# Optimization experiments

Measured on AMD Instinct MI355X. Metric: run time of the kernel, lower is better.

The kernel has to match this reference:

```python
import jax, jax.numpy as jnp
import numpy as np

C = 256
CQK = C // 8  # query/key channels


def setup_inputs() -> dict:
    key = jax.random.key(0)
    ks = jax.random.split(key, 7)
    B, H, W = 4, 64, 64
    x = jax.random.normal(ks[0], (B, C, H, W), dtype=jnp.float32)
    # 1x1 conv weights stored as [out_ch, in_ch] (kernel spatial dims are 1)
    sc = 1.0 / np.sqrt(C)
    Wq = jax.random.uniform(ks[1], (CQK, C), jnp.float32, -sc, sc)
    bq = jax.random.uniform(ks[2], (CQK,), jnp.float32, -sc, sc)
    Wk = jax.random.uniform(ks[3], (CQK, C), jnp.float32, -sc, sc)
    bk = jax.random.uniform(ks[4], (CQK,), jnp.float32, -sc, sc)
    Wv = jax.random.uniform(ks[5], (C, C), jnp.float32, -sc, sc)
    bv = jax.random.uniform(ks[6], (C,), jnp.float32, -sc, sc)
    gamma = jnp.zeros((1,), dtype=jnp.float32)
    return {"x": x, "Wq": Wq, "bq": bq, "Wk": Wk, "bk": bk, "Wv": Wv, "bv": bv, "gamma": gamma}


def reference(x, Wq, bq, Wk, bk, Wv, bv, gamma):
    B, Ch, H, W = x.shape
    N = H * W
    xf = x.reshape(B, Ch, N)  # [B, C, N]
    # 1x1 convs == per-pixel linear projections
    q = jnp.einsum('oc,bcn->bno', Wq, xf) + bq  # [B, N, CQK]
    k = jnp.einsum('oc,bcn->bon', Wk, xf) + bk[None, :, None]  # [B, CQK, N]
    v = jnp.einsum('oc,bcn->bon', Wv, xf) + bv[None, :, None]  # [B, C, N]
    s = jnp.einsum('bnd,bdm->bnm', q, k)  # [B, N, N]
    attn = jax.nn.softmax(s, axis=-1)
    # out[b,c,i] = sum_j v[b,c,j] * attn[b,i,j]
    out = jnp.einsum('bcj,bij->bci', v, attn).reshape(B, Ch, H, W)
    return x + gamma[0] * out
```

## Files before the change

kernel.cpp:

```cpp
#include <hip/hip_runtime.h>
#include <math.h>

#define BATCH 4
#define CCH   256
#define DQK   32
#define NPIX  4096
#define LOG2E 1.44269504088896340736f

typedef __attribute__((ext_vector_type(8)))  short          short8_t;
typedef __attribute__((ext_vector_type(4)))  unsigned short ushort4_t;
typedef __attribute__((ext_vector_type(8)))  unsigned short ushort8_t;
typedef __attribute__((ext_vector_type(16))) float          f32x16;
typedef __attribute__((ext_vector_type(2)))  unsigned int   uint2_t;

#if __has_builtin(__builtin_amdgcn_exp2f)
#define EXP2F(x) __builtin_amdgcn_exp2f(x)
#else
#define EXP2F(x) exp2f(x)
#endif

#define MFMA32(a, b, c) __builtin_amdgcn_mfma_f32_32x32x16_bf16(a, b, c, 0, 0, 0)

static __device__ __forceinline__ unsigned short f2bf(float f) {
    union { float f; unsigned int u; } v; v.f = f;
    unsigned int r = v.u + 0x7FFFu + ((v.u >> 16) & 1u);
    return (unsigned short)(r >> 16);
}

static __device__ __forceinline__ short8_t cat8(ushort4_t a, ushort4_t b) {
    ushort8_t c = __builtin_shufflevector(a, b, 0, 1, 2, 3, 4, 5, 6, 7);
    short8_t r; __builtin_memcpy(&r, &c, 16); return r;
}

static __device__ __forceinline__ short8_t u4_to_s8(const unsigned int* u) {
    short8_t r; __builtin_memcpy(&r, u, 16); return r;
}

static __device__ __forceinline__ uint2_t plswap(unsigned int a, unsigned int b) {
#if __has_builtin(__builtin_amdgcn_permlane32_swap)
    return __builtin_amdgcn_permlane32_swap(a, b, false, false);
#else
    const unsigned int sa = (unsigned int)__shfl_xor((int)a, 32);
    const unsigned int sb = (unsigned int)__shfl_xor((int)b, 32);
    const int h = (threadIdx.x >> 5) & 1;
    uint2_t r;
    r.x = h ? sb : a;
    r.y = h ? b : sa;
    return r;
#endif
}

static __device__ __forceinline__ void make_bfrag(
    const f32x16& s, float& l0, float& l1, unsigned int bfr[2][4])
{
    float pv[16];
    #pragma unroll
    for (int r = 0; r < 16; ++r) pv[r] = EXP2F(s[r]);
    #pragma unroll
    for (int r = 0; r < 16; r += 2) { l0 += pv[r]; l1 += pv[r + 1]; }
    unsigned int P[8];
    #pragma unroll
    for (int v = 0; v < 8; ++v)
        P[v] = __builtin_amdgcn_perm(__float_as_uint(pv[2 * v + 1]),
                                     __float_as_uint(pv[2 * v]), 0x07060302u);
    #pragma unroll
    for (int kp = 0; kp < 2; ++kp) {
        const uint2_t r02 = plswap(P[4 * kp + 0], P[4 * kp + 2]);
        const uint2_t r13 = plswap(P[4 * kp + 1], P[4 * kp + 3]);
        bfr[kp][0] = r02.x; bfr[kp][1] = r13.x;
        bfr[kp][2] = r02.y; bfr[kp][3] = r13.y;
    }
}

__global__ __launch_bounds__(256) void wconv_kernel(
    const float* __restrict__ Wq, const float* __restrict__ Wk,
    const float* __restrict__ Wv, unsigned short* __restrict__ wbf)
{
    const int idx = blockIdx.x * 256 + threadIdx.x;
    const int o = idx >> 8, c = idx & 255;
    float v;
    if (o < 32)      v = Wq[o * 256 + c] * LOG2E;
    else if (o < 64) v = Wk[(o - 32) * 256 + c];
    else             v = Wv[(o - 64) * 256 + c];
    wbf[((c >> 3) * 320 + o) * 8 + (c & 7)] = f2bf(v);
}

__global__ __launch_bounds__(256) void xt_kernel(
    const float* __restrict__ x, unsigned short* __restrict__ xfrag)
{
    const int b  = blockIdx.x >> 6;
    const int cg = (blockIdx.x >> 4) & 3;
    const int ng = blockIdx.x & 15;
    const int t  = threadIdx.x;
    const int w = t >> 6, l = t & 63;

    #pragma unroll
    for (int sgl = 0; sgl < 2; ++sgl) {
        const int sg = w * 2 + sgl;
        float f[4][8];
        #pragma unroll
        for (int p = 0; p < 8; ++p) {
            const float* row = x + ((size_t)(b * CCH + cg * 64 + sg * 8 + p)) * NPIX
                                 + ng * 256;
            #pragma unroll
            for (int j = 0; j < 4; ++j)
                f[j][p] = row[j * 64 + l];
        }
        #pragma unroll
        for (int j = 0; j < 4; ++j) {
            unsigned int d[4];
            #pragma unroll
            for (int k = 0; k < 4; ++k)
                d[k] = __builtin_amdgcn_perm(__float_as_uint(f[j][2 * k + 1]),
                                             __float_as_uint(f[j][2 * k]), 0x07060302u);
            const int nt = ng * 8 + j * 2 + (l >> 5);
            unsigned short* dst = xfrag +
                ((((size_t)(b * 128 + nt) * 32) + cg * 8 + sg) * 32 + (l & 31)) * 8;
            *(short8_t*)dst = u4_to_s8(d);
        }
    }
}

__global__ __launch_bounds__(320) void proj_kernel(
    const unsigned short* __restrict__ xfrag, const unsigned short* __restrict__ wbf,
    const float* __restrict__ bq, const float* __restrict__ bk,
    const float* __restrict__ bv,
    unsigned short* __restrict__ qfrag, unsigned short* __restrict__ kfrag,
    unsigned short* __restrict__ vfrag)
{
    __shared__ unsigned short qkb[2 * 2 * 32 * 40];
    __shared__ unsigned short vbuf[4 * 64 * 72];

    const int b   = blockIdx.x >> 6;
    const int nt0 = (blockIdx.x & 63) << 1;
    const int t   = threadIdx.x;
    const int w = t >> 6, lane = t & 63, il = lane & 31, h = lane >> 5;

    float4 bA[4], bB[4];
    #pragma unroll
    for (int g = 0; g < 4; ++g) {
        if (w == 0) {
            bA[g] = *(const float4*)&bq[8 * g + 4 * h];
            bB[g] = *(const float4*)&bk[8 * g + 4 * h];
        } else {
            bA[g] = *(const float4*)&bv[(w - 1) * 64 + 8 * g + 4 * h];
            bB[g] = *(const float4*)&bv[(w - 1) * 64 + 32 + 8 * g + 4 * h];
        }
    }

    f32x16 acc[2][2];
    #pragma unroll
    for (int a = 0; a < 2; ++a)
        #pragma unroll
        for (int i = 0; i < 2; ++i)
            #pragma unroll
            for (int r = 0; r < 16; ++r) acc[a][i][r] = 0.f;

    const unsigned short* wp = wbf + ((size_t)(h * 320 + w * 64 + il)) * 8;
    const unsigned short* xp0 = xfrag + (((size_t)(b * 128 + nt0) * 32 + h) * 32 + il) * 8;
    const unsigned short* xp1 = xp0 + (size_t)32 * 32 * 8;

    #pragma unroll 4
    for (int ks = 0; ks < 16; ++ks) {
        const short8_t af0 = *(const short8_t*)(wp + ks * 5120);
        const short8_t af1 = *(const short8_t*)(wp + ks * 5120 + 256);
        const short8_t bf0 = *(const short8_t*)(xp0 + (size_t)ks * 2 * 256);
        const short8_t bf1 = *(const short8_t*)(xp1 + (size_t)ks * 2 * 256);
        acc[0][0] = MFMA32(af0, bf0, acc[0][0]);
        acc[0][1] = MFMA32(af0, bf1, acc[0][1]);
        acc[1][0] = MFMA32(af1, bf0, acc[1][0]);
        acc[1][1] = MFMA32(af1, bf1, acc[1][1]);
    }

    if (w == 0) {
        #pragma unroll
        for (int it = 0; it < 2; ++it)
            #pragma unroll
            for (int r = 0; r < 16; ++r) {
                const int d = (r & 3) + 8 * (r >> 2) + 4 * h;
                qkb[(it * 2 + 0) * 1280 + il * 40 + d] =
                    f2bf(acc[0][it][r] + bA[r >> 2][r & 3] * LOG2E);
                qkb[(it * 2 + 1) * 1280 + il * 40 + d] =
                    f2bf(acc[1][it][r] + bB[r >> 2][r & 3]);
            }
        #pragma unroll
        for (int it = 0; it < 2; ++it)
            #pragma unroll
            for (int rep = 0; rep < 2; ++rep) {
                const int u = rep * 64 + lane;
                const int slot = u >> 5, n = u & 31;
                ushort4_t qlo = *(const ushort4_t*)&qkb[(it * 2) * 1280 + n * 40 + slot * 8];
                ushort4_t qhi = *(const ushort4_t*)&qkb[(it * 2) * 1280 + n * 40 + slot * 8 + 4];
                ushort4_t klo = *(const ushort4_t*)&qkb[(it * 2 + 1) * 1280 + n * 40 + slot * 8];
                ushort4_t khi = *(const ushort4_t*)&qkb[(it * 2 + 1) * 1280 + n * 40 + slot * 8 + 4];
                const size_t o8 = (((size_t)(b * 128 + nt0 + it) * 4 + slot) * 32 + n) * 8;
                *(short8_t*)(qfrag + o8) = cat8(qlo, qhi);
                *(short8_t*)(kfrag + o8) = cat8(klo, khi);
            }
    } else {
        unsigned short* vb = vbuf + (w - 1) * 64 * 72;
        #pragma unroll
        for (int it = 0; it < 2; ++it)
            #pragma unroll
            for (int r = 0; r < 16; ++r) {
                const int orow = (r & 3) + 8 * (r >> 2) + 4 * h;
                vb[(orow)      * 72 + it * 32 + il] = f2bf(acc[0][it][r] + bA[r >> 2][r & 3]);
                vb[(orow + 32) * 72 + it * 32 + il] = f2bf(acc[1][it][r] + bB[r >> 2][r & 3]);
            }
        #pragma unroll
        for (int rep = 0; rep < 8; ++rep) {
            const int u = rep * 64 + lane;
            const int c = u & 63, m = u >> 6;
            const int it = m >> 2, slot = m & 3;
            ushort4_t lo = *(const ushort4_t*)&vb[c * 72 + it * 32 + slot * 8];
            ushort4_t hi = *(const ushort4_t*)&vb[c * 72 + it * 32 + slot * 8 + 4];
            const size_t o8 = (((size_t)(b * 128 + nt0 + it) * 4 + slot) * 256 +
                               (w - 1) * 64 + c) * 8;
            *(short8_t*)(vfrag + o8) = cat8(lo, hi);
        }
    }
}

struct KStage { short8_t k0, k1; };

__global__ __launch_bounds__(512, 2) void attn_kernel(
    const unsigned short* __restrict__ qfrag,
    const unsigned short* __restrict__ kfrag,
    const unsigned short* __restrict__ vfrag,
    const float* __restrict__ x,
    const float* __restrict__ gamma,
    float* __restrict__ out)
{
    __shared__ float comb[8][64][17];

    const int m8 = blockIdx.x & 7;
    const int b  = m8 >> 1;
    const int itile = ((blockIdx.x >> 3) << 1) | (m8 & 1);
    const int i0 = itile << 6;
    const int t  = threadIdx.x;
    const int w = t >> 6, lane = t & 63, il = lane & 31, h = lane >> 5;
    const int it = w & 1, ci = (w >> 1) & 1, jj = w >> 2;

    short8_t qf[2];
    #pragma unroll
    for (int ks = 0; ks < 2; ++ks)
        qf[ks] = *(const short8_t*)(qfrag +
            (((size_t)(b * 128 + itile * 2 + it) * 4 + ks * 2 + h) * 32 + il) * 8);

    const size_t kbase = (size_t)(b * 128 + jj * 64) * 1024 + h * 256 + il * 8;
    const size_t vbase = (size_t)(b * 128 + jj * 64) * 8192 + h * 2048 +
                         (ci * 128 + il) * 8;

    f32x16 zf;
    #pragma unroll
    for (int r = 0; r < 16; ++r) zf[r] = 0.f;
    f32x16 acc[4];
    #pragma unroll
    for (int c4 = 0; c4 < 4; ++c4) acc[c4] = zf;
    float ls[2] = {0.f, 0.f};

    KStage A, B;
    short8_t va[4][2], vb[4][2];

    auto loadK = [&](KStage& S, int jt) {
        const unsigned short* kp = kfrag + kbase + (size_t)jt * 1024;
        S.k0 = *(const short8_t*)kp;
        S.k1 = *(const short8_t*)(kp + 512);
    };
    auto loadV = [&](short8_t (&vv)[4][2], int jt) {
        const unsigned short* vp = vfrag + vbase + (size_t)jt * 8192;
        #pragma unroll
        for (int ct = 0; ct < 4; ++ct) {
            vv[ct][0] = *(const short8_t*)(vp + ct * 256);
            vv[ct][1] = *(const short8_t*)(vp + ct * 256 + 4096);
        }
    };

    loadK(A, 0);
    loadK(B, 1);
    f32x16 sA = MFMA32(A.k0, qf[0], zf);
    sA = MFMA32(A.k1, qf[1], sA);
    f32x16 sB = MFMA32(B.k0, qf[0], zf);
    sB = MFMA32(B.k1, qf[1], sB);
    loadK(A, 2);
    loadK(B, 3);
    loadV(va, 0);
    loadV(vb, 1);

    #pragma unroll 1
    for (int jt = 0; jt < 64; jt += 2) {
        unsigned int bfA[2][4];
        make_bfrag(sA, ls[0], ls[1], bfA);
        sA = MFMA32(A.k0, qf[0], zf);
        sA = MFMA32(A.k1, qf[1], sA);
        if (jt + 4 < 64) loadK(A, jt + 4);
        __builtin_amdgcn_s_setprio(1);
        #pragma unroll
        for (int ct = 0; ct < 4; ++ct) {
            acc[ct] = MFMA32(va[ct][0], u4_to_s8(bfA[0]), acc[ct]);
            acc[ct] = MFMA32(va[ct][1], u4_to_s8(bfA[1]), acc[ct]);
        }
        __builtin_amdgcn_s_setprio(0);
        if (jt + 2 < 64) loadV(va, jt + 2);

        unsigned int bfB[2][4];
        make_bfrag(sB, ls[0], ls[1], bfB);
        sB = MFMA32(B.k0, qf[0], zf);
        sB = MFMA32(B.k1, qf[1], sB);
        if (jt + 5 < 64) loadK(B, jt + 5);
        __builtin_amdgcn_s_setprio(1);
        #pragma unroll
        for (int ct = 0; ct < 4; ++ct) {
            acc[ct] = MFMA32(vb[ct][0], u4_to_s8(bfB[0]), acc[ct]);
            acc[ct] = MFMA32(vb[ct][1], u4_to_s8(bfB[1]), acc[ct]);
        }
        __builtin_amdgcn_s_setprio(0);
        if (jt + 3 < 64) loadV(vb, jt + 3);
    }

    float l = ls[0] + ls[1];
    l += __shfl_xor(l, 32);
    const float gam = gamma[0];
    const int pw = w ^ 4;
    float lt = 0.f;

    #pragma unroll
    for (int ct = 0; ct < 4; ++ct) {
        __syncthreads();
        #pragma unroll
        for (int r = 0; r < 16; ++r) comb[w][lane][r] = acc[ct][r];
        if (ct == 0) comb[w][lane][16] = l;
        __syncthreads();
        if (ct == 0) lt = l + comb[pw][lane][16];
        if ((ct >> 1) == jj) {
            const float sc = gam / lt;
            #pragma unroll
            for (int r = 0; r < 16; ++r) {
                const float o = acc[ct][r] + comb[pw][lane][r];
                const int c = ci * 128 + ct * 32 + (r & 3) + 8 * (r >> 2) + 4 * h;
                const size_t idx = ((size_t)(b * CCH + c)) * NPIX + i0 +
                                   it * 32 + il;
                out[idx] = x[idx] + o * sc;
            }
        }
    }
}

extern "C" void kernel_launch(void* const* d_in, const int* in_sizes, int n_in,
                              void* d_out, int out_size, void* d_ws, size_t ws_size,
                              hipStream_t stream) {
    const float* x     = (const float*)d_in[0];
    const float* Wq    = (const float*)d_in[1];
    const float* bq    = (const float*)d_in[2];
    const float* Wk    = (const float*)d_in[3];
    const float* bk    = (const float*)d_in[4];
    const float* Wv    = (const float*)d_in[5];
    const float* bv    = (const float*)d_in[6];
    const float* gamma = (const float*)d_in[7];
    float* out = (float*)d_out;

    unsigned short* ws    = (unsigned short*)d_ws;
    unsigned short* wbf   = ws;
    unsigned short* xfrag = ws + 81920;
    unsigned short* qfrag = xfrag + (size_t)4194304;
    unsigned short* kfrag = qfrag + (size_t)524288;
    unsigned short* vfrag = kfrag + (size_t)524288;

    wconv_kernel<<<dim3(320), dim3(256), 0, stream>>>(Wq, Wk, Wv, wbf);
    xt_kernel<<<dim3(256), dim3(256), 0, stream>>>(x, xfrag);
    proj_kernel<<<dim3(256), dim3(320), 0, stream>>>(
        xfrag, wbf, bq, bk, bv, qfrag, kfrag, vfrag);
    attn_kernel<<<dim3(256), dim3(512), 0, stream>>>(
        qfrag, kfrag, vfrag, x, gamma, out);
}
```

Before: 150.7 us.

## Fuse x transpose/bf16 conversion into projection kernel via shared memory staging

Result: faster. 146.8 us, median of 3 (-2.6%).

```diff
diff --git a/kernel.cpp b/kernel.cpp
--- a/kernel.cpp
+++ b/kernel.cpp
@@ -85,56 +85,33 @@
     wbf[((c >> 3) * 320 + o) * 8 + (c & 7)] = f2bf(v);
 }
 
-__global__ __launch_bounds__(256) void xt_kernel(
-    const float* __restrict__ x, unsigned short* __restrict__ xfrag)
-{
-    const int b  = blockIdx.x >> 6;
-    const int cg = (blockIdx.x >> 4) & 3;
-    const int ng = blockIdx.x & 15;
-    const int t  = threadIdx.x;
-    const int w = t >> 6, l = t & 63;
-
-    #pragma unroll
-    for (int sgl = 0; sgl < 2; ++sgl) {
-        const int sg = w * 2 + sgl;
-        float f[4][8];
-        #pragma unroll
-        for (int p = 0; p < 8; ++p) {
-            const float* row = x + ((size_t)(b * CCH + cg * 64 + sg * 8 + p)) * NPIX
-                                 + ng * 256;
-            #pragma unroll
-            for (int j = 0; j < 4; ++j)
-                f[j][p] = row[j * 64 + l];
-        }
-        #pragma unroll
-        for (int j = 0; j < 4; ++j) {
-            unsigned int d[4];
-            #pragma unroll
-            for (int k = 0; k < 4; ++k)
-                d[k] = __builtin_amdgcn_perm(__float_as_uint(f[j][2 * k + 1]),
-                                             __float_as_uint(f[j][2 * k]), 0x07060302u);
-            const int nt = ng * 8 + j * 2 + (l >> 5);
-            unsigned short* dst = xfrag +
-                ((((size_t)(b * 128 + nt) * 32) + cg * 8 + sg) * 32 + (l & 31)) * 8;
-            *(short8_t*)dst = u4_to_s8(d);
-        }
-    }
-}
-
-__global__ __launch_bounds__(320) void proj_kernel(
-    const unsigned short* __restrict__ xfrag, const unsigned short* __restrict__ wbf,
+__global__ __launch_bounds__(320) void xtproj_kernel(
+    const float* __restrict__ x, const unsigned short* __restrict__ wbf,
     const float* __restrict__ bq, const float* __restrict__ bk,
     const float* __restrict__ bv,
     unsigned short* __restrict__ qfrag, unsigned short* __restrict__ kfrag,
     unsigned short* __restrict__ vfrag)
 {
+    __shared__ unsigned short xls[2][32][32][8];
     __shared__ unsigned short qkb[2 * 2 * 32 * 40];
     __shared__ unsigned short vbuf[4 * 64 * 72];
 
     const int b   = blockIdx.x >> 6;
     const int nt0 = (blockIdx.x & 63) << 1;
+    const int n0  = nt0 << 5;
     const int t   = threadIdx.x;
     const int w = t >> 6, lane = t & 63, il = lane & 31, h = lane >> 5;
+
+    for (int q = t; q < 4096; q += 320) {
+        const int c  = q >> 4;
+        const int n4 = (q & 15) << 2;
+        const float4 f = *(const float4*)&x[((size_t)(b * CCH + c)) * NPIX + n0 + n4];
+        unsigned short* dst = &xls[n4 >> 5][c >> 3][n4 & 31][c & 7];
+        dst[0]  = f2bf(f.x);
+        dst[8]  = f2bf(f.y);
+        dst[16] = f2bf(f.z);
+        dst[24] = f2bf(f.w);
+    }
 
     float4 bA[4], bB[4];
     #pragma unroll
@@ -156,16 +133,16 @@
             #pragma unroll
             for (int r = 0; r < 16; ++r) acc[a][i][r] = 0.f;
 
+    __syncthreads();
+
     const unsigned short* wp = wbf + ((size_t)(h * 320 + w * 64 + il)) * 8;
-    const unsigned short* xp0 = xfrag + (((size_t)(b * 128 + nt0) * 32 + h) * 32 + il) * 8;
-    const unsigned short* xp1 = xp0 + (size_t)32 * 32 * 8;
 
     #pragma unroll 4
     for (int ks = 0; ks < 16; ++ks) {
         const short8_t af0 = *(const short8_t*)(wp + ks * 5120);
         const short8_t af1 = *(const short8_t*)(wp + ks * 5120 + 256);
-        const short8_t bf0 = *(const short8_t*)(xp0 + (size_t)ks * 2 * 256);
-        const short8_t bf1 = *(const short8_t*)(xp1 + (size_t)ks * 2 * 256);
+        const short8_t bf0 = *(const short8_t*)&xls[0][2 * ks + h][il][0];
+        const short8_t bf1 = *(const short8_t*)&xls[1][2 * ks + h][il][0];
         acc[0][0] = MFMA32(af0, bf0, acc[0][0]);
         acc[0][1] = MFMA32(af0, bf1, acc[0][1]);
         acc[1][0] = MFMA32(af1, bf0, acc[1][0]);
@@ -361,15 +338,13 @@
 
     unsigned short* ws    = (unsigned short*)d_ws;
     unsigned short* wbf   = ws;
-    unsigned short* xfrag = ws + 81920;
-    unsigned short* qfrag = xfrag + (size_t)4194304;
+    unsigned short* qfrag = ws + 81920;
     unsigned short* kfrag = qfrag + (size_t)524288;
     unsigned short* vfrag = kfrag + (size_t)524288;
 
     wconv_kernel<<<dim3(320), dim3(256), 0, stream>>>(Wq, Wk, Wv, wbf);
-    xt_kernel<<<dim3(256), dim3(256), 0, stream>>>(x, xfrag);
-    proj_kernel<<<dim3(256), dim3(320), 0, stream>>>(
-        xfrag, wbf, bq, bk, bv, qfrag, kfrag, vfrag);
+    xtproj_kernel<<<dim3(256), dim3(320), 0, stream>>>(
+        x, wbf, bq, bk, bv, qfrag, kfrag, vfrag);
     attn_kernel<<<dim3(256), dim3(512), 0, stream>>>(
         qfrag, kfrag, vfrag, x, gamma, out);
 }
```
